# Optimization experiments

Measured on AMD Instinct MI355X. Metric: run time of the kernel, lower is better.

Reference implementation:

```python
import jax, jax.numpy as jnp
import numpy as np

HEADS = 8
DIM_HEAD = 128
EPS = 1e-5


def layer_norm(t, gamma):
    mu = jnp.mean(t, axis=-1, keepdims=True)
    var = jnp.var(t, axis=-1, keepdims=True)
    return (t - mu) / jnp.sqrt(var + EPS) * gamma


def setup_inputs() -> dict:
    key = jax.random.key(0)
    k1, k2, k3 = jax.random.split(key, 3)
    B, N, T, D = 16, 256, 4096, 1024
    img_queries = jax.random.normal(k1, (B, N, D), dtype=jnp.float32)
    x = jax.random.normal(k2, (B, T, D), dtype=jnp.float32)
    gamma_q = jnp.ones((D,), dtype=jnp.float32)
    gamma_x = jnp.ones((D,), dtype=jnp.float32)
    W_kv = jax.random.normal(k3, (D, 2 * DIM_HEAD), dtype=jnp.float32) * 0.02
    return {"img_queries": img_queries, "x": x, "gamma_q": gamma_q,
            "gamma_x": gamma_x, "W_kv": W_kv}


def reference(img_queries, x, gamma_q, gamma_x, W_kv):
    B, N, D = img_queries.shape
    scale = DIM_HEAD ** -0.5
    q_n = layer_norm(img_queries, gamma_q)            # [B,N,D]
    x_n = layer_norm(x, gamma_x)                      # [B,T,D]
    # b n (h d) -> b h n d
    q = q_n.reshape(B, N, HEADS, DIM_HEAD).transpose(0, 2, 1, 3)
    kv = x_n @ W_kv                                   # [B,T,2*dim_head]
    k = kv[..., :DIM_HEAD]                            # shared single K head; v chunk unused
    sim = jnp.einsum('bhid,bjd->bhij', q * scale, k)  # [B,H,N,T]
    sim = sim - jnp.max(sim, axis=-1, keepdims=True)
    attn = jax.nn.softmax(sim, axis=-1)
    out = jnp.einsum('bhij,bjf->bhif', attn, x_n)     # V = raw normed x, [B,H,N,D]
    # b h n f -> b (n h f)
    out = out.transpose(0, 2, 1, 3).reshape(B, N * HEADS * D)
    return out, attn
```

## Files before the change

### kernel.cpp

```cpp
#include <hip/hip_runtime.h>

typedef unsigned short u16;
typedef unsigned int u32;
typedef __attribute__((ext_vector_type(8))) short short8;
typedef __attribute__((ext_vector_type(4))) float f32x4;
typedef __attribute__((ext_vector_type(4))) unsigned int u32x4;

#define SCALE 0.08838834764831845f
#define OUT_ELEMS 33554432ull

__device__ __forceinline__ u16 f2b(float f) {
  u32 u = __float_as_uint(f);
  u32 r = u + 0x7fffu + ((u >> 16) & 1u);
  return (u16)(r >> 16);
}

__device__ __forceinline__ u32 cvtpk(float lo, float hi) {
  u32 r;
  asm("v_cvt_pk_bf16_f32 %0, %1, %2" : "=v"(r) : "v"(lo), "v"(hi));
  return r;
}

__device__ __forceinline__ void gload16(const void* g, void* l) {
  __builtin_amdgcn_global_load_lds((const __attribute__((address_space(1))) void*)g,
                                   (__attribute__((address_space(3))) void*)l, 16, 0, 0);
}

__device__ __forceinline__ uint2 shflx2(uint2 v, int m) {
  uint2 r;
  r.x = __shfl_xor(v.x, m, 64);
  r.y = __shfl_xor(v.y, m, 64);
  return r;
}

__global__ __launch_bounds__(256) void ln_rows(const float* __restrict__ in,
                                               const float* __restrict__ gamma,
                                               u16* __restrict__ out, float scale) {
  const int row = blockIdx.x;
  const int t = threadIdx.x;
  const float4 v = *(const float4*)(in + (size_t)row * 1024 + t * 4);
  float s = v.x + v.y + v.z + v.w;
  float q = v.x * v.x + v.y * v.y + v.z * v.z + v.w * v.w;
#pragma unroll
  for (int m = 32; m; m >>= 1) {
    s += __shfl_down(s, m);
    q += __shfl_down(q, m);
  }
  __shared__ float red[8];
  const int w = t >> 6;
  if ((t & 63) == 0) { red[w] = s; red[4 + w] = q; }
  __syncthreads();
  s = red[0] + red[1] + red[2] + red[3];
  q = red[4] + red[5] + red[6] + red[7];
  const float mu = s * (1.0f / 1024.0f);
  const float var = q * (1.0f / 1024.0f) - mu * mu;
  const float rs = rsqrtf(var + 1e-5f) * scale;
  const float4 g = *(const float4*)(gamma + t * 4);
  ushort4 o;
  o.x = f2b((v.x - mu) * rs * g.x);
  o.y = f2b((v.y - mu) * rs * g.y);
  o.z = f2b((v.z - mu) * rs * g.z);
  o.w = f2b((v.w - mu) * rs * g.w);
  *(ushort4*)(out + (size_t)row * 1024 + t * 4) = o;
}

__global__ __launch_bounds__(256) void cvt_w(const float* __restrict__ w, u16* __restrict__ wt) {
  const int n = blockIdx.x;
  const int t = threadIdx.x;
  const int d = t * 4;
  ushort4 o;
  o.x = f2b(w[(size_t)(d + 0) * 256 + n]);
  o.y = f2b(w[(size_t)(d + 1) * 256 + n]);
  o.z = f2b(w[(size_t)(d + 2) * 256 + n]);
  o.w = f2b(w[(size_t)(d + 3) * 256 + n]);
  *(ushort4*)(wt + (size_t)n * 1024 + d) = o;
}

__global__ __launch_bounds__(256) void transpose_xn(const u16* __restrict__ xn,
                                                    u16* __restrict__ xnt) {
  const int jt = blockIdx.x, dt = blockIdx.y, b = blockIdx.z;
  __shared__ u16 tile[64][72];
  const int t = threadIdx.x;
  const size_t src = ((size_t)b * 4096 + jt * 64) * 1024 + dt * 64;
#pragma unroll
  for (int p = 0; p < 2; ++p) {
    const int idx = t + 256 * p;
    const int j = idx >> 3, c = idx & 7;
    *(short8*)(&tile[j][c * 8]) = *(const short8*)(xn + src + (size_t)j * 1024 + c * 8);
  }
  __syncthreads();
  const size_t dst = ((size_t)b * 1024 + dt * 64) * 4096 + jt * 64;
#pragma unroll
  for (int p = 0; p < 2; ++p) {
    const int idx = t + 256 * p;
    const int d = idx >> 3, jj = idx & 7;
    short8 o;
#pragma unroll
    for (int e = 0; e < 8; ++e) o[e] = (short)tile[jj * 8 + e][d];
    *(short8*)(xnt + dst + (size_t)d * 4096 + jj * 8) = o;
  }
}

__global__ __launch_bounds__(256) void kgemm(const u16* __restrict__ xn,
                                             const u16* __restrict__ wt,
                                             u16* __restrict__ ks) {
  __shared__ u16 As[128 * 32];
  __shared__ u16 Bs[128 * 32];
  const int t = threadIdx.x;
  const int lane = t & 63, w = t >> 6;
  const int wm = w >> 1, wn = w & 1;
  const int j0 = blockIdx.x * 128;
  const int g = lane >> 4, r16 = lane & 15;
  f32x4 acc[4][4] = {};
  for (int k0 = 0; k0 < 1024; k0 += 32) {
    __syncthreads();
#pragma unroll
    for (int i = 0; i < 2; ++i) {
      const int seg = i * 4 + w;
      const int off = seg * 1024 + lane * 16;
      const int row = off >> 6;
      const int c = (off >> 4) & 3;
      const int sw = c ^ ((row >> 1) & 3);
      gload16(xn + ((size_t)(j0 + row)) * 1024 + k0 + sw * 8, (char*)As + seg * 1024);
      gload16(wt + ((size_t)row) * 1024 + k0 + sw * 8, (char*)Bs + seg * 1024);
    }
    __syncthreads();
    short8 a[4], bq[4];
#pragma unroll
    for (int mt = 0; mt < 4; ++mt) {
      const int row = wm * 64 + mt * 16 + r16;
      const int sw = g ^ ((row >> 1) & 3);
      a[mt] = *(const short8*)(As + row * 32 + sw * 8);
    }
#pragma unroll
    for (int nt = 0; nt < 4; ++nt) {
      const int row = wn * 64 + nt * 16 + r16;
      const int sw = g ^ ((row >> 1) & 3);
      bq[nt] = *(const short8*)(Bs + row * 32 + sw * 8);
    }
#pragma unroll
    for (int mt = 0; mt < 4; ++mt)
#pragma unroll
      for (int nt = 0; nt < 4; ++nt)
        acc[mt][nt] = __builtin_amdgcn_mfma_f32_16x16x32_bf16(a[mt], bq[nt], acc[mt][nt], 0, 0, 0);
  }
#pragma unroll
  for (int mt = 0; mt < 4; ++mt)
#pragma unroll
    for (int nt = 0; nt < 4; ++nt)
#pragma unroll
      for (int r = 0; r < 4; ++r) {
        const int j = j0 + wm * 64 + mt * 16 + g * 4 + r;
        const int n = wn * 64 + nt * 16 + r16;
        ks[(size_t)j * 128 + n] = f2b(acc[mt][nt][r]);
      }
}

__global__ __launch_bounds__(1024) void attn_kernel(const u16* __restrict__ qs,
                                                    const u16* __restrict__ ks,
                                                    u16* __restrict__ attnb) {
  const int orig = blockIdx.x;
  const int blk = (orig & 7) * 256 + (orig >> 3);
  const int it = blk & 15, h = (blk >> 4) & 7, b = blk >> 7;
  const int i0 = it * 16;
  const int t = threadIdx.x;
  const int lane = t & 63, w = t >> 6;
  const int g = lane >> 4, r16 = lane & 15;
  __shared__ u16 Q[16 * 128];
  __shared__ float redm[256];
  __shared__ float reds[256];
  if (t < 256) {
    const int row = t >> 4, c = t & 15;
    const int sw = c ^ (row & 7);
    *(short8*)(Q + row * 128 + sw * 8) =
        *(const short8*)(qs + ((size_t)(b * 256 + i0 + row)) * 1024 + h * 128 + c * 8);
  }
  __syncthreads();
  short8 a[4];
#pragma unroll
  for (int kp = 0; kp < 4; ++kp) {
    const int c = kp * 4 + g;
    const int sw = c ^ (r16 & 7);
    a[kp] = *(const short8*)(Q + r16 * 128 + sw * 8);
  }
  const u16* kb = ks + (size_t)b * 4096 * 128;
  const int j0 = w * 256;
  f32x4 acc[16] = {};
#pragma unroll
  for (int kp = 0; kp < 4; ++kp) {
#pragma unroll
    for (int nt = 0; nt < 16; ++nt) {
      const short8 bv = *(const short8*)(kb + (size_t)(j0 + nt * 16 + r16) * 128 + kp * 32 + g * 8);
      acc[nt] = __builtin_amdgcn_mfma_f32_16x16x32_bf16(bv, a[kp], acc[nt], 0, 0, 0);
    }
  }
  float mx = acc[0][0];
#pragma unroll
  for (int nt = 0; nt < 16; ++nt)
#pragma unroll
    for (int r = 0; r < 4; ++r) mx = fmaxf(mx, acc[nt][r]);
  mx = fmaxf(mx, __shfl_xor(mx, 16));
  mx = fmaxf(mx, __shfl_xor(mx, 32));
  if (lane < 16) redm[w * 16 + lane] = mx;
  __syncthreads();
  float m = redm[r16];
#pragma unroll
  for (int w2 = 1; w2 < 16; ++w2) m = fmaxf(m, redm[w2 * 16 + r16]);
  float sm = 0.f;
#pragma unroll
  for (int nt = 0; nt < 16; ++nt)
#pragma unroll
    for (int r = 0; r < 4; ++r) {
      const float p = __expf(acc[nt][r] - m);
      acc[nt][r] = p;
      sm += p;
    }
  sm += __shfl_xor(sm, 16);
  sm += __shfl_xor(sm, 32);
  if (lane < 16) reds[w * 16 + lane] = sm;
  __syncthreads();
  float s = reds[r16];
#pragma unroll
  for (int w2 = 1; w2 < 16; ++w2) s += reds[w2 * 16 + r16];
  const float inv = 1.0f / s;
#pragma unroll
  for (int nt = 0; nt < 16; ++nt) acc[nt] *= inv;

  u16* brow = attnb + ((size_t)((b * 8 + h) * 256 + i0 + r16)) * 4096 + j0;
  const bool gb0 = (g & 1), gb1 = (g & 2);
#pragma unroll
  for (int q4 = 0; q4 < 4; ++q4) {
    uint2 X[4];
#pragma unroll
    for (int i = 0; i < 4; ++i) {
      const f32x4 v = acc[q4 * 4 + i];
      X[i] = make_uint2(cvtpk(v[0], v[1]), cvtpk(v[2], v[3]));
    }
#pragma unroll
    for (int k = 0; k < 2; ++k) {
      const uint2 aa = X[2 * k], bb = X[2 * k + 1];
      const uint2 sent = gb0 ? aa : bb;
      const uint2 recv = shflx2(sent, 16);
      X[2 * k] = gb0 ? recv : aa;
      X[2 * k + 1] = gb0 ? bb : recv;
    }
#pragma unroll
    for (int k = 0; k < 2; ++k) {
      const uint2 aa = X[k], bb = X[k + 2];
      const uint2 sent = gb1 ? aa : bb;
      const uint2 recv = shflx2(sent, 32);
      X[k] = gb1 ? recv : aa;
      X[k + 2] = gb1 ? bb : recv;
    }
    u16* bp = brow + q4 * 64 + g * 16;
    u32x4 o0 = {X[0].x, X[0].y, X[1].x, X[1].y};
    u32x4 o1 = {X[2].x, X[2].y, X[3].x, X[3].y};
    *(u32x4*)bp = o0;
    *(u32x4*)(bp + 8) = o1;
  }
}

__global__ __launch_bounds__(512, 2) void ogemm256(const u16* __restrict__ attnb,
                                                   const u16* __restrict__ xnt,
                                                   float* __restrict__ out,
                                                   float* __restrict__ attn) {
  extern __shared__ u16 S[];
  const int orig = blockIdx.x;
  const int wid = (orig & 7) * 64 + (orig >> 3);
  const int b = wid >> 5, ft = (wid >> 3) & 3, h = wid & 7;
  const int t = threadIdx.x;
  const int lane = t & 63, w = t >> 6;
  const int wm = w >> 2, wn = w & 3;
  const int g = lane >> 4, r16 = lane & 15;
  const u16* Ab = attnb + ((size_t)(b * 8 + h) * 256) * 4096;
  const u16* Bb = xnt + ((size_t)b * 1024 + ft * 256) * 4096;
  const bool wrA = (ft == 0);
  float* attn_out = attn + ((size_t)(b * 8 + h) * 256) * 4096;
  const int wr_base = w * 4 + (lane >> 4);
  const int wc16 = lane & 15;
  const int wchunk = wc16 >> 1;
  const int whalf = (wc16 & 1) * 8;

  int srow[4], scol[4];
#pragma unroll
  for (int seg = 0; seg < 4; ++seg) {
    const int gi = seg * 512 + t;
    srow[seg] = gi >> 3;
    scol[seg] = (((gi & 7) ^ ((gi >> 3) & 7)) * 8);
  }
  const int wuni = w * 1024;

#define OSTAGE(buf, k0)                                                         \
  do {                                                                          \
    _Pragma("unroll") for (int seg = 0; seg < 4; ++seg)                         \
        gload16(Ab + (size_t)srow[seg] * 4096 + (k0) + scol[seg],               \
                (char*)S + (buf)*32768 + seg * 8192 + wuni);                    \
    _Pragma("unroll") for (int seg = 0; seg < 4; ++seg)                         \
        gload16(Bb + (size_t)srow[seg] * 4096 + (k0) + scol[seg],               \
                (char*)S + 65536 + (buf)*32768 + seg * 8192 + wuni);            \
  } while (0)

  f32x4 acc[8][4] = {};
  OSTAGE(0, 0);
  OSTAGE(1, 64);
  asm volatile("s_waitcnt vmcnt(8)" ::: "memory");
  __builtin_amdgcn_s_barrier();

  for (int t64 = 0; t64 < 64; ++t64) {
    const int buf = t64 & 1;
    const char* A0 = (const char*)S + buf * 32768;
    const char* B0 = (const char*)S + 65536 + buf * 32768;
    short8 af[8], bf[4];
#pragma unroll
    for (int mt = 0; mt < 8; ++mt) {
      const int row = wm * 128 + mt * 16 + r16;
      af[mt] = *(const short8*)(A0 + row * 128 + ((g ^ (row & 7)) * 16));
    }
#pragma unroll
    for (int nt = 0; nt < 4; ++nt) {
      const int row = wn * 64 + nt * 16 + r16;
      bf[nt] = *(const short8*)(B0 + row * 128 + ((g ^ (row & 7)) * 16));
    }
    asm volatile("s_waitcnt lgkmcnt(0)" ::: "memory");
    __builtin_amdgcn_sched_barrier(0);
    __builtin_amdgcn_s_setprio(1);
#pragma unroll
    for (int mt = 0; mt < 8; ++mt)
#pragma unroll
      for (int nt = 0; nt < 4; ++nt)
        acc[mt][nt] = __builtin_amdgcn_mfma_f32_16x16x32_bf16(af[mt], bf[nt], acc[mt][nt], 0, 0, 0);
    __builtin_amdgcn_s_setprio(0);
#pragma unroll
    for (int mt = 0; mt < 8; ++mt) {
      const int row = wm * 128 + mt * 16 + r16;
      af[mt] = *(const short8*)(A0 + row * 128 + (((4 + g) ^ (row & 7)) * 16));
    }
#pragma unroll
    for (int nt = 0; nt < 4; ++nt) {
      const int row = wn * 64 + nt * 16 + r16;
      bf[nt] = *(const short8*)(B0 + row * 128 + (((4 + g) ^ (row & 7)) * 16));
    }
    uint2 wv[8];
    if (wrA) {
#pragma unroll
      for (int s = 0; s < 8; ++s) {
        const int row = s * 32 + wr_base;
        wv[s] = *(const uint2*)(A0 + row * 128 + ((wchunk ^ (row & 7)) * 16) + whalf);
      }
    }
    asm volatile("s_waitcnt lgkmcnt(0)" ::: "memory");
    __builtin_amdgcn_sched_barrier(0);
    if (wrA) {
#pragma unroll
      for (int s = 0; s < 8; ++s) {
        const int row = s * 32 + wr_base;
        f32x4 o;
        o[0] = __uint_as_float(wv[s].x << 16);
        o[1] = __uint_as_float(wv[s].x & 0xffff0000u);
        o[2] = __uint_as_float(wv[s].y << 16);
        o[3] = __uint_as_float(wv[s].y & 0xffff0000u);
        __builtin_nontemporal_store(o, (f32x4*)(attn_out + (size_t)row * 4096 + t64 * 64 + wc16 * 4));
      }
      __builtin_amdgcn_sched_barrier(0);
    }
    __builtin_amdgcn_s_barrier();
    if (t64 + 2 < 64) OSTAGE(buf, (t64 + 2) * 64);
    __builtin_amdgcn_s_setprio(1);
#pragma unroll
    for (int mt = 0; mt < 8; ++mt)
#pragma unroll
      for (int nt = 0; nt < 4; ++nt)
        acc[mt][nt] = __builtin_amdgcn_mfma_f32_16x16x32_bf16(af[mt], bf[nt], acc[mt][nt], 0, 0, 0);
    __builtin_amdgcn_s_setprio(0);
    if (t64 + 2 < 64) {
      if (wrA)
        asm volatile("s_waitcnt vmcnt(16)" ::: "memory");
      else
        asm volatile("s_waitcnt vmcnt(8)" ::: "memory");
    } else if (t64 == 62) {
      asm volatile("s_waitcnt vmcnt(0)" ::: "memory");
    }
    __builtin_amdgcn_s_barrier();
  }
#undef OSTAGE

  float* ob = out + (size_t)b * 2097152 + (size_t)h * 1024;
#pragma unroll
  for (int mt = 0; mt < 8; ++mt)
#pragma unroll
    for (int nt = 0; nt < 4; ++nt)
#pragma unroll
      for (int r = 0; r < 4; ++r) {
        const int i = wm * 128 + mt * 16 + g * 4 + r;
        const int f = ft * 256 + wn * 64 + nt * 16 + r16;
        ob[(size_t)i * 8192 + f] = acc[mt][nt][r];
      }
}

extern "C" void kernel_launch(void* const* d_in, const int* in_sizes, int n_in,
                              void* d_out, int out_size, void* d_ws, size_t ws_size,
                              hipStream_t stream) {
  const float* img_q = (const float*)d_in[0];
  const float* x = (const float*)d_in[1];
  const float* gamma_q = (const float*)d_in[2];
  const float* gamma_x = (const float*)d_in[3];
  const float* wkv = (const float*)d_in[4];

  float* out_f = (float*)d_out;
  float* attn_f = out_f + OUT_ELEMS;

  u16* xn = (u16*)attn_f;
  u16* qsb = (u16*)out_f;
  u16* wtb = qsb + 4194304;
  u16* ksb = wtb + 131072;
  u16* xnt = (u16*)d_ws;
  u16* attnb = xnt + 67108864;

  if (ws_size < (size_t)402653184) return;

  (void)hipFuncSetAttribute((const void*)ogemm256,
                            hipFuncAttributeMaxDynamicSharedMemorySize, 131072);

  ln_rows<<<65536, 256, 0, stream>>>(x, gamma_x, xn, 1.0f);
  ln_rows<<<4096, 256, 0, stream>>>(img_q, gamma_q, qsb, SCALE);
  cvt_w<<<128, 256, 0, stream>>>(wkv, wtb);
  transpose_xn<<<dim3(64, 16, 16), 256, 0, stream>>>(xn, xnt);
  kgemm<<<512, 256, 0, stream>>>(xn, wtb, ksb);
  attn_kernel<<<2048, 1024, 0, stream>>>(qsb, ksb, attnb);
  ogemm256<<<512, 512, 131072, stream>>>(attnb, xnt, out_f, attn_f);
}
```

Measured before the change: 846.5 us.

## Fuse x layernorm with transpose and software-pipeline LDS fragment reads in ogemm

A new ln_xpose kernel normalizes 32 rows of x per block and writes both the row-major bf16 xn and its transpose xnt from a shared tile. This removes the separate transpose kernel and its extra read of xn. The output GEMM's inner loop now loads A fragments in halves and interleaves the LDS reads with MFMA groups using partial lgkmcnt waits. It also prefetches the next buffer's fragments after the barrier, aiming to hide LDS latency and cut register pressure. The risks are a 64 KB LDS tile limiting ln_xpose occupancy and the xnt stores being 16-byte writes with a 8 KB stride.

Measured after the change: 839.6 us. Within noise of the previous version (-0.8%).

```diff
diff --git a/kernel.cpp b/kernel.cpp
--- a/kernel.cpp
+++ b/kernel.cpp
@@ -64,6 +64,72 @@
   *(ushort4*)(out + (size_t)row * 1024 + t * 4) = o;
 }
 
+__global__ __launch_bounds__(1024) void ln_xpose(const float* __restrict__ in,
+                                                 const float* __restrict__ gamma,
+                                                 u16* __restrict__ xn,
+                                                 u16* __restrict__ xnt) {
+  __shared__ u16 tile[32][1024];
+  const int blk = blockIdx.x;
+  const int b = blk >> 7;
+  const int jj0 = (blk & 127) * 32;
+  const int t = threadIdx.x;
+  const int lane = t & 63, w = t >> 6;
+  const size_t j0 = (size_t)blk * 32;
+
+  float4 gv[4];
+#pragma unroll
+  for (int k = 0; k < 4; ++k) gv[k] = *(const float4*)(gamma + k * 256 + lane * 4);
+
+  float4 va[2][4];
+  float mu[2], rs[2];
+#pragma unroll
+  for (int rr = 0; rr < 2; ++rr) {
+    const int row = w * 2 + rr;
+    const float* src = in + (j0 + row) * 1024;
+    float s = 0.f, q = 0.f;
+#pragma unroll
+    for (int k = 0; k < 4; ++k) {
+      const float4 v = *(const float4*)(src + k * 256 + lane * 4);
+      va[rr][k] = v;
+      s += v.x + v.y + v.z + v.w;
+      q += v.x * v.x + v.y * v.y + v.z * v.z + v.w * v.w;
+    }
+#pragma unroll
+    for (int m = 1; m < 64; m <<= 1) {
+      s += __shfl_xor(s, m);
+      q += __shfl_xor(q, m);
+    }
+    const float m_ = s * (1.0f / 1024.0f);
+    mu[rr] = m_;
+    rs[rr] = rsqrtf(q * (1.0f / 1024.0f) - m_ * m_ + 1e-5f);
+  }
+#pragma unroll
+  for (int rr = 0; rr < 2; ++rr) {
+    const int row = w * 2 + rr;
+    u16* xrow = xn + (j0 + row) * 1024;
+#pragma unroll
+    for (int k = 0; k < 4; ++k) {
+      const float4 v = va[rr][k];
+      uint2 p;
+      p.x = cvtpk((v.x - mu[rr]) * rs[rr] * gv[k].x, (v.y - mu[rr]) * rs[rr] * gv[k].y);
+      p.y = cvtpk((v.z - mu[rr]) * rs[rr] * gv[k].z, (v.w - mu[rr]) * rs[rr] * gv[k].w);
+      *(uint2*)(xrow + k * 256 + lane * 4) = p;
+      *(uint2*)(&tile[row][k * 256 + lane * 4]) = p;
+    }
+  }
+  __syncthreads();
+  u32 o[16];
+#pragma unroll
+  for (int r = 0; r < 16; ++r)
+    o[r] = (u32)tile[2 * r][t] | ((u32)tile[2 * r + 1][t] << 16);
+  u16* dst = xnt + ((size_t)b * 1024 + t) * 4096 + jj0;
+#pragma unroll
+  for (int k = 0; k < 4; ++k) {
+    u32x4 v = {o[4 * k + 0], o[4 * k + 1], o[4 * k + 2], o[4 * k + 3]};
+    *(u32x4*)(dst + k * 8) = v;
+  }
+}
+
 __global__ __launch_bounds__(256) void cvt_w(const float* __restrict__ w, u16* __restrict__ wt) {
   const int n = blockIdx.x;
   const int t = threadIdx.x;
@@ -74,31 +140,6 @@
   o.z = f2b(w[(size_t)(d + 2) * 256 + n]);
   o.w = f2b(w[(size_t)(d + 3) * 256 + n]);
   *(ushort4*)(wt + (size_t)n * 1024 + d) = o;
-}
-
-__global__ __launch_bounds__(256) void transpose_xn(const u16* __restrict__ xn,
-                                                    u16* __restrict__ xnt) {
-  const int jt = blockIdx.x, dt = blockIdx.y, b = blockIdx.z;
-  __shared__ u16 tile[64][72];
-  const int t = threadIdx.x;
-  const size_t src = ((size_t)b * 4096 + jt * 64) * 1024 + dt * 64;
-#pragma unroll
-  for (int p = 0; p < 2; ++p) {
-    const int idx = t + 256 * p;
-    const int j = idx >> 3, c = idx & 7;
-    *(short8*)(&tile[j][c * 8]) = *(const short8*)(xn + src + (size_t)j * 1024 + c * 8);
-  }
-  __syncthreads();
-  const size_t dst = ((size_t)b * 1024 + dt * 64) * 4096 + jt * 64;
-#pragma unroll
-  for (int p = 0; p < 2; ++p) {
-    const int idx = t + 256 * p;
-    const int d = idx >> 3, jj = idx & 7;
-    short8 o;
-#pragma unroll
-    for (int e = 0; e < 8; ++e) o[e] = (short)tile[jj * 8 + e][d];
-    *(short8*)(xnt + dst + (size_t)d * 4096 + jj * 8) = o;
-  }
 }
 
 __global__ __launch_bounds__(256) void kgemm(const u16* __restrict__ xn,
@@ -300,46 +341,64 @@
                 (char*)S + 65536 + (buf)*32768 + seg * 8192 + wuni);            \
   } while (0)
 
+#define AFRD(dstv, A0p, half, ks)                                               \
+  do {                                                                          \
+    _Pragma("unroll") for (int mt = 0; mt < 4; ++mt) {                          \
+      const int row = wm * 128 + ((half)*4 + mt) * 16 + r16;                    \
+      dstv[mt] = *(const short8*)((A0p) + row * 128 + ((((ks)*4 + g) ^ (row & 7)) * 16)); \
+    }                                                                           \
+  } while (0)
+
+#define BFRD(dstv, B0p, ks)                                                     \
+  do {                                                                          \
+    _Pragma("unroll") for (int nt = 0; nt < 4; ++nt) {                          \
+      const int row = wn * 64 + nt * 16 + r16;                                  \
+      dstv[nt] = *(const short8*)((B0p) + row * 128 + ((((ks)*4 + g) ^ (row & 7)) * 16)); \
+    }                                                                           \
+  } while (0)
+
+#define MFMA16(base, av, bv)                                                    \
+  do {                                                                          \
+    __builtin_amdgcn_s_setprio(1);                                              \
+    _Pragma("unroll") for (int mt = 0; mt < 4; ++mt)                            \
+      _Pragma("unroll") for (int nt = 0; nt < 4; ++nt)                          \
+        acc[(base) + mt][nt] =                                                  \
+            __builtin_amdgcn_mfma_f32_16x16x32_bf16(av[mt], bv[nt], acc[(base) + mt][nt], 0, 0, 0); \
+    __builtin_amdgcn_s_setprio(0);                                              \
+    __builtin_amdgcn_sched_barrier(0);                                          \
+  } while (0)
+
   f32x4 acc[8][4] = {};
   OSTAGE(0, 0);
   OSTAGE(1, 64);
   asm volatile("s_waitcnt vmcnt(8)" ::: "memory");
   __builtin_amdgcn_s_barrier();
 
+  short8 af[4], an[4], bf[4];
+  BFRD(bf, (const char*)S + 65536, 0);
+  AFRD(af, (const char*)S, 0, 0);
+
   for (int t64 = 0; t64 < 64; ++t64) {
     const int buf = t64 & 1;
     const char* A0 = (const char*)S + buf * 32768;
     const char* B0 = (const char*)S + 65536 + buf * 32768;
-    short8 af[8], bf[4];
-#pragma unroll
-    for (int mt = 0; mt < 8; ++mt) {
-      const int row = wm * 128 + mt * 16 + r16;
-      af[mt] = *(const short8*)(A0 + row * 128 + ((g ^ (row & 7)) * 16));
-    }
-#pragma unroll
-    for (int nt = 0; nt < 4; ++nt) {
-      const int row = wn * 64 + nt * 16 + r16;
-      bf[nt] = *(const short8*)(B0 + row * 128 + ((g ^ (row & 7)) * 16));
-    }
-    asm volatile("s_waitcnt lgkmcnt(0)" ::: "memory");
+
+    AFRD(an, A0, 1, 0);
+    asm volatile("s_waitcnt lgkmcnt(4)" ::: "memory");
     __builtin_amdgcn_sched_barrier(0);
-    __builtin_amdgcn_s_setprio(1);
-#pragma unroll
-    for (int mt = 0; mt < 8; ++mt)
-#pragma unroll
-      for (int nt = 0; nt < 4; ++nt)
-        acc[mt][nt] = __builtin_amdgcn_mfma_f32_16x16x32_bf16(af[mt], bf[nt], acc[mt][nt], 0, 0, 0);
-    __builtin_amdgcn_s_setprio(0);
-#pragma unroll
-    for (int mt = 0; mt < 8; ++mt) {
-      const int row = wm * 128 + mt * 16 + r16;
-      af[mt] = *(const short8*)(A0 + row * 128 + (((4 + g) ^ (row & 7)) * 16));
-    }
-#pragma unroll
-    for (int nt = 0; nt < 4; ++nt) {
-      const int row = wn * 64 + nt * 16 + r16;
-      bf[nt] = *(const short8*)(B0 + row * 128 + (((4 + g) ^ (row & 7)) * 16));
-    }
+    MFMA16(0, af, bf);
+
+    AFRD(af, A0, 0, 1);
+    asm volatile("s_waitcnt lgkmcnt(4)" ::: "memory");
+    __builtin_amdgcn_sched_barrier(0);
+    MFMA16(4, an, bf);
+
+    BFRD(bf, B0, 1);
+    AFRD(an, A0, 1, 1);
+    asm volatile("s_waitcnt lgkmcnt(4)" ::: "memory");
+    __builtin_amdgcn_sched_barrier(0);
+    MFMA16(0, af, bf);
+
     uint2 wv[8];
     if (wrA) {
 #pragma unroll
@@ -347,10 +406,16 @@
         const int row = s * 32 + wr_base;
         wv[s] = *(const uint2*)(A0 + row * 128 + ((wchunk ^ (row & 7)) * 16) + whalf);
       }
-    }
-    asm volatile("s_waitcnt lgkmcnt(0)" ::: "memory");
+      asm volatile("s_waitcnt lgkmcnt(8)" ::: "memory");
+    } else {
+      asm volatile("s_waitcnt lgkmcnt(0)" ::: "memory");
+    }
     __builtin_amdgcn_sched_barrier(0);
+    MFMA16(4, an, bf);
+
     if (wrA) {
+      asm volatile("s_waitcnt lgkmcnt(0)" ::: "memory");
+      __builtin_amdgcn_sched_barrier(0);
 #pragma unroll
       for (int s = 0; s < 8; ++s) {
         const int row = s * 32 + wr_base;
@@ -365,24 +430,26 @@
     }
     __builtin_amdgcn_s_barrier();
     if (t64 + 2 < 64) OSTAGE(buf, (t64 + 2) * 64);
-    __builtin_amdgcn_s_setprio(1);
-#pragma unroll
-    for (int mt = 0; mt < 8; ++mt)
-#pragma unroll
-      for (int nt = 0; nt < 4; ++nt)
-        acc[mt][nt] = __builtin_amdgcn_mfma_f32_16x16x32_bf16(af[mt], bf[nt], acc[mt][nt], 0, 0, 0);
-    __builtin_amdgcn_s_setprio(0);
     if (t64 + 2 < 64) {
       if (wrA)
         asm volatile("s_waitcnt vmcnt(16)" ::: "memory");
       else
         asm volatile("s_waitcnt vmcnt(8)" ::: "memory");
-    } else if (t64 == 62) {
+    } else {
       asm volatile("s_waitcnt vmcnt(0)" ::: "memory");
     }
     __builtin_amdgcn_s_barrier();
+    if (t64 + 1 < 64) {
+      const char* A1 = (const char*)S + (buf ^ 1) * 32768;
+      const char* B1 = (const char*)S + 65536 + (buf ^ 1) * 32768;
+      BFRD(bf, B1, 0);
+      AFRD(af, A1, 0, 0);
+    }
   }
 #undef OSTAGE
+#undef AFRD
+#undef BFRD
+#undef MFMA16
 
   float* ob = out + (size_t)b * 2097152 + (size_t)h * 1024;
 #pragma unroll
@@ -421,10 +488,9 @@
   (void)hipFuncSetAttribute((const void*)ogemm256,
                             hipFuncAttributeMaxDynamicSharedMemorySize, 131072);
 
-  ln_rows<<<65536, 256, 0, stream>>>(x, gamma_x, xn, 1.0f);
+  ln_xpose<<<2048, 1024, 0, stream>>>(x, gamma_x, xn, xnt);
   ln_rows<<<4096, 256, 0, stream>>>(img_q, gamma_q, qsb, SCALE);
   cvt_w<<<128, 256, 0, stream>>>(wkv, wtb);
-  transpose_xn<<<dim3(64, 16, 16), 256, 0, stream>>>(xn, xnt);
   kgemm<<<512, 256, 0, stream>>>(xn, wtb, ksb);
   attn_kernel<<<2048, 1024, 0, stream>>>(qsb, ksb, attnb);
   ogemm256<<<512, 512, 131072, stream>>>(attnb, xnt, out_f, attn_f);
```

## Fuse x layernorm with transpose and use single-pass softmax reduction

Applied to the files above, without the earlier changes.

Replaces the separate layernorm and transpose kernels for x with one kernel that normalizes 32 rows per block, writes the row-major bf16 copy, and writes the transposed copy through shared memory. This avoids re-reading the 128 MB bf16 xn for the transpose and removes one launch. The attention softmax now computes each wave's local max and exp-sum together and merges them with rescaling, so one block barrier replaces two. It adds extra exp calls for the rescale, and the transpose tile is a 64 KB LDS buffer at 1024 threads per block.

Result: faster. 817.0 us (median of 2 runs) (-3.5%).

```diff
diff --git a/kernel.cpp b/kernel.cpp
--- a/kernel.cpp
+++ b/kernel.cpp
@@ -64,6 +64,72 @@
   *(ushort4*)(out + (size_t)row * 1024 + t * 4) = o;
 }
 
+__global__ __launch_bounds__(1024) void ln_xpose(const float* __restrict__ in,
+                                                 const float* __restrict__ gamma,
+                                                 u16* __restrict__ xn,
+                                                 u16* __restrict__ xnt) {
+  __shared__ u16 tile[32][1024];
+  const int blk = blockIdx.x;
+  const int b = blk >> 7;
+  const int jj0 = (blk & 127) * 32;
+  const int t = threadIdx.x;
+  const int lane = t & 63, w = t >> 6;
+  const size_t j0 = (size_t)blk * 32;
+
+  float4 gv[4];
+#pragma unroll
+  for (int k = 0; k < 4; ++k) gv[k] = *(const float4*)(gamma + k * 256 + lane * 4);
+
+  float4 va[2][4];
+  float mu[2], rs[2];
+#pragma unroll
+  for (int rr = 0; rr < 2; ++rr) {
+    const int row = w * 2 + rr;
+    const float* src = in + (j0 + row) * 1024;
+    float s = 0.f, q = 0.f;
+#pragma unroll
+    for (int k = 0; k < 4; ++k) {
+      const float4 v = *(const float4*)(src + k * 256 + lane * 4);
+      va[rr][k] = v;
+      s += v.x + v.y + v.z + v.w;
+      q += v.x * v.x + v.y * v.y + v.z * v.z + v.w * v.w;
+    }
+#pragma unroll
+    for (int m = 1; m < 64; m <<= 1) {
+      s += __shfl_xor(s, m);
+      q += __shfl_xor(q, m);
+    }
+    const float m_ = s * (1.0f / 1024.0f);
+    mu[rr] = m_;
+    rs[rr] = rsqrtf(q * (1.0f / 1024.0f) - m_ * m_ + 1e-5f);
+  }
+#pragma unroll
+  for (int rr = 0; rr < 2; ++rr) {
+    const int row = w * 2 + rr;
+    u16* xrow = xn + (j0 + row) * 1024;
+#pragma unroll
+    for (int k = 0; k < 4; ++k) {
+      const float4 v = va[rr][k];
+      uint2 p;
+      p.x = cvtpk((v.x - mu[rr]) * rs[rr] * gv[k].x, (v.y - mu[rr]) * rs[rr] * gv[k].y);
+      p.y = cvtpk((v.z - mu[rr]) * rs[rr] * gv[k].z, (v.w - mu[rr]) * rs[rr] * gv[k].w);
+      *(uint2*)(xrow + k * 256 + lane * 4) = p;
+      *(uint2*)(&tile[row][k * 256 + lane * 4]) = p;
+    }
+  }
+  __syncthreads();
+  u32 o[16];
+#pragma unroll
+  for (int r = 0; r < 16; ++r)
+    o[r] = (u32)tile[2 * r][t] | ((u32)tile[2 * r + 1][t] << 16);
+  u16* dst = xnt + ((size_t)b * 1024 + t) * 4096 + jj0;
+#pragma unroll
+  for (int k = 0; k < 4; ++k) {
+    u32x4 v = {o[4 * k + 0], o[4 * k + 1], o[4 * k + 2], o[4 * k + 3]};
+    *(u32x4*)(dst + k * 8) = v;
+  }
+}
+
 __global__ __launch_bounds__(256) void cvt_w(const float* __restrict__ w, u16* __restrict__ wt) {
   const int n = blockIdx.x;
   const int t = threadIdx.x;
@@ -74,31 +140,6 @@
   o.z = f2b(w[(size_t)(d + 2) * 256 + n]);
   o.w = f2b(w[(size_t)(d + 3) * 256 + n]);
   *(ushort4*)(wt + (size_t)n * 1024 + d) = o;
-}
-
-__global__ __launch_bounds__(256) void transpose_xn(const u16* __restrict__ xn,
-                                                    u16* __restrict__ xnt) {
-  const int jt = blockIdx.x, dt = blockIdx.y, b = blockIdx.z;
-  __shared__ u16 tile[64][72];
-  const int t = threadIdx.x;
-  const size_t src = ((size_t)b * 4096 + jt * 64) * 1024 + dt * 64;
-#pragma unroll
-  for (int p = 0; p < 2; ++p) {
-    const int idx = t + 256 * p;
-    const int j = idx >> 3, c = idx & 7;
-    *(short8*)(&tile[j][c * 8]) = *(const short8*)(xn + src + (size_t)j * 1024 + c * 8);
-  }
-  __syncthreads();
-  const size_t dst = ((size_t)b * 1024 + dt * 64) * 4096 + jt * 64;
-#pragma unroll
-  for (int p = 0; p < 2; ++p) {
-    const int idx = t + 256 * p;
-    const int d = idx >> 3, jj = idx & 7;
-    short8 o;
-#pragma unroll
-    for (int e = 0; e < 8; ++e) o[e] = (short)tile[jj * 8 + e][d];
-    *(short8*)(xnt + dst + (size_t)d * 4096 + jj * 8) = o;
-  }
 }
 
 __global__ __launch_bounds__(256) void kgemm(const u16* __restrict__ xn,
@@ -201,30 +242,32 @@
     for (int r = 0; r < 4; ++r) mx = fmaxf(mx, acc[nt][r]);
   mx = fmaxf(mx, __shfl_xor(mx, 16));
   mx = fmaxf(mx, __shfl_xor(mx, 32));
-  if (lane < 16) redm[w * 16 + lane] = mx;
+  float sm = 0.f;
+#pragma unroll
+  for (int nt = 0; nt < 16; ++nt)
+#pragma unroll
+    for (int r = 0; r < 4; ++r) {
+      const float p = __expf(acc[nt][r] - mx);
+      acc[nt][r] = p;
+      sm += p;
+    }
+  sm += __shfl_xor(sm, 16);
+  sm += __shfl_xor(sm, 32);
+  if (lane < 16) {
+    redm[w * 16 + lane] = mx;
+    reds[w * 16 + lane] = sm;
+  }
   __syncthreads();
   float m = redm[r16];
 #pragma unroll
   for (int w2 = 1; w2 < 16; ++w2) m = fmaxf(m, redm[w2 * 16 + r16]);
-  float sm = 0.f;
-#pragma unroll
-  for (int nt = 0; nt < 16; ++nt)
-#pragma unroll
-    for (int r = 0; r < 4; ++r) {
-      const float p = __expf(acc[nt][r] - m);
-      acc[nt][r] = p;
-      sm += p;
-    }
-  sm += __shfl_xor(sm, 16);
-  sm += __shfl_xor(sm, 32);
-  if (lane < 16) reds[w * 16 + lane] = sm;
-  __syncthreads();
-  float s = reds[r16];
-#pragma unroll
-  for (int w2 = 1; w2 < 16; ++w2) s += reds[w2 * 16 + r16];
-  const float inv = 1.0f / s;
-#pragma unroll
-  for (int nt = 0; nt < 16; ++nt) acc[nt] *= inv;
+  float s = 0.f;
+#pragma unroll
+  for (int w2 = 0; w2 < 16; ++w2)
+    s += reds[w2 * 16 + r16] * __expf(redm[w2 * 16 + r16] - m);
+  const float f = __expf(mx - m) / s;
+#pragma unroll
+  for (int nt = 0; nt < 16; ++nt) acc[nt] *= f;
 
   u16* brow = attnb + ((size_t)((b * 8 + h) * 256 + i0 + r16)) * 4096 + j0;
   const bool gb0 = (g & 1), gb1 = (g & 2);
@@ -421,10 +464,9 @@
   (void)hipFuncSetAttribute((const void*)ogemm256,
                             hipFuncAttributeMaxDynamicSharedMemorySize, 131072);
 
-  ln_rows<<<65536, 256, 0, stream>>>(x, gamma_x, xn, 1.0f);
+  ln_xpose<<<2048, 1024, 0, stream>>>(x, gamma_x, xn, xnt);
   ln_rows<<<4096, 256, 0, stream>>>(img_q, gamma_q, qsb, SCALE);
   cvt_w<<<128, 256, 0, stream>>>(wkv, wtb);
-  transpose_xn<<<dim3(64, 16, 16), 256, 0, stream>>>(xn, xnt);
   kgemm<<<512, 256, 0, stream>>>(xn, wtb, ksb);
   attn_kernel<<<2048, 1024, 0, stream>>>(qsb, ksb, attnb);
   ogemm256<<<512, 512, 131072, stream>>>(attnb, xnt, out_f, attn_f);
```
